# Optimization experiments

Hardware: AMD Instinct MI355X
Metric: run time of the kernel (lower is better)

The kernel has to match this reference:

```python
import jax, jax.numpy as jnp
import numpy as np

HIDDEN = 1024
NUM_QUBITS = 16
QUBIT_DIM = 64  # HIDDEN == NUM_QUBITS * QUBIT_DIM
LN_EPS = 1e-6   # flax nn.LayerNorm default


def setup_inputs() -> dict:
    key = jax.random.key(0)
    k_x, k_w = jax.random.split(key)
    B, S = 4, 4096
    x = jax.random.normal(k_x, (B, S, HIDDEN), dtype=jnp.float32)
    # Learned params (flax defaults: LN scale=ones, bias=zeros; Dense lecun_normal kernel, zero bias)
    ln_scale = jnp.ones((HIDDEN,), dtype=jnp.float32)
    ln_bias = jnp.zeros((HIDDEN,), dtype=jnp.float32)
    dense_w = jax.random.normal(k_w, (HIDDEN, HIDDEN), dtype=jnp.float32) * (1.0 / np.sqrt(HIDDEN))
    dense_b = jnp.zeros((HIDDEN,), dtype=jnp.float32)
    return {"x": x, "ln_scale": ln_scale, "ln_bias": ln_bias,
            "dense_w": dense_w, "dense_b": dense_b}


def reference(x, ln_scale, ln_bias, dense_w, dense_b):
    B, S, H = x.shape
    # input_preparation: LayerNorm over last axis, then reshape (B,S,Q,D)
    mean = jnp.mean(x, axis=-1, keepdims=True)
    var = jnp.mean(jnp.square(x - mean), axis=-1, keepdims=True)
    h = (x - mean) * jax.lax.rsqrt(var + LN_EPS) * ln_scale + ln_bias
    h = h.reshape(B, S, NUM_QUBITS, QUBIT_DIM)
    # quantum_forward (default jax backend): sin*cos, FFT along qubit axis, real part
    h = jnp.sin(h) * jnp.cos(h)
    h = jnp.real(jnp.fft.fft(h.astype(jnp.complex64), axis=-2))
    # post_process: restore (B,S,H) then Dense(hidden_size)
    h = h.reshape(B, S, H)
    return jnp.einsum('bsh,hk->bsk', h, dense_w) + dense_b
```

## Files before the change

### kernel.cpp

```cpp
#include <hip/hip_runtime.h>
#include <hip/hip_bf16.h>

#define HID 1024
#define NQ 16
#define QD 64
#define MROWS 16384

typedef __bf16 bf16;
typedef __bf16 bf16x8 __attribute__((ext_vector_type(8)));
typedef __bf16 bf16x4 __attribute__((ext_vector_type(4)));
typedef float f32x4 __attribute__((ext_vector_type(4)));

__global__ __launch_bounds__(256) void wt_k(const float* __restrict__ W,
                                            bf16* __restrict__ Wt) {
    int idx = blockIdx.x * 256 + threadIdx.x;
    int n = idx >> 6;
    int d = idx & 63;

    float w[16];
#pragma unroll
    for (int qp = 0; qp < 16; ++qp)
        w[qp] = W[(size_t)(qp * QD + d) * HID + n];

    const float ct[16] = {
        1.0f,  0.92387953f,  0.70710678f,  0.38268343f,
        0.0f, -0.38268343f, -0.70710678f, -0.92387953f,
       -1.0f, -0.92387953f, -0.70710678f, -0.38268343f,
        0.0f,  0.38268343f,  0.70710678f,  0.92387953f};

#pragma unroll
    for (int q = 0; q < 16; ++q) {
        float acc = 0.0f;
#pragma unroll
        for (int qp = 0; qp < 16; ++qp)
            acc += w[qp] * ct[(q * qp) & 15];
        Wt[(size_t)n * HID + q * QD + d] = (bf16)acc;
    }
}

__global__ __launch_bounds__(256) void prep_k(const float* __restrict__ x,
                                              const float* __restrict__ gamma,
                                              const float* __restrict__ beta,
                                              bf16* __restrict__ A) {
    int row = blockIdx.x;
    int t = threadIdx.x;
    const float4* xr = (const float4*)(x + (size_t)row * HID);
    float4 v = xr[t];

    float s  = v.x + v.y + v.z + v.w;
    float ss = v.x * v.x + v.y * v.y + v.z * v.z + v.w * v.w;
#pragma unroll
    for (int off = 32; off; off >>= 1) {
        s  += __shfl_down(s, off);
        ss += __shfl_down(ss, off);
    }
    __shared__ float red[8];
    int wv = t >> 6, ln = t & 63;
    if (ln == 0) { red[wv] = s; red[4 + wv] = ss; }
    __syncthreads();
    float Sm = red[0] + red[1] + red[2] + red[3];
    float Ss = red[4] + red[5] + red[6] + red[7];
    float mean = Sm * (1.0f / HID);
    float var  = Ss * (1.0f / HID) - mean * mean;
    float rstd = rsqrtf(var + 1e-6f);

    float4 g = ((const float4*)gamma)[t];
    float4 b = ((const float4*)beta)[t];

    float h0 = (v.x - mean) * rstd * g.x + b.x;
    float h1 = (v.y - mean) * rstd * g.y + b.y;
    float h2 = (v.z - mean) * rstd * g.z + b.z;
    float h3 = (v.w - mean) * rstd * g.w + b.w;

    bf16x4 o;
    o[0] = (bf16)(0.5f * __sinf(2.0f * h0));
    o[1] = (bf16)(0.5f * __sinf(2.0f * h1));
    o[2] = (bf16)(0.5f * __sinf(2.0f * h2));
    o[3] = (bf16)(0.5f * __sinf(2.0f * h3));
    ((bf16x4*)(A + (size_t)row * HID))[t] = o;
}

#define BM 256
#define BN 256
#define BK 64
#define NT (HID / BK)

#define MFMA(va, vb, vc) __builtin_amdgcn_mfma_f32_16x16x32_bf16(va, vb, vc, 0, 0, 0)

__global__ __launch_bounds__(512, 2) void gemm_k(const bf16* __restrict__ A,
                                                 const bf16* __restrict__ Bt,
                                                 const float* __restrict__ bias,
                                                 float* __restrict__ C) {
    __shared__ __attribute__((aligned(16))) char lds[131072];

    const int tid = threadIdx.x;
    const int w = tid >> 6, ln = tid & 63;
    const int wm = w >> 2, wn = w & 3;
    const int fr = ln & 15, fq = ln >> 4;

    int orig = blockIdx.x;
    int wg = (orig & 7) * 32 + (orig >> 3);
    int bm = wg >> 2, bn = wg & 3;

    const bf16* Ab = A + (size_t)bm * BM * HID;
    const bf16* Bb = Bt + (size_t)bn * BN * HID;

    auto stage = [&](int buf, int mat, int R0, int kt) {
        const char* gsrc = (const char*)(mat ? Bb : Ab);
        char* base = lds + (((buf << 1) | mat) << 15) + (R0 << 7);
        const int kb = kt << 7;
#pragma unroll
        for (int l = 0; l < 2; ++l) {
            int c = (l << 9) + tid;
            int lr = c >> 3;
            int colB = ((c & 7) ^ (lr & 7)) << 4;
            const char* g = gsrc + (size_t)(R0 + lr) * (HID * 2) + kb + colB;
            __builtin_amdgcn_global_load_lds(
                (const __attribute__((address_space(1))) void*)g,
                (__attribute__((address_space(3))) void*)(base + (((l << 9) + (w << 6)) << 4)),
                16, 0, 0);
        }
    };

    auto readA = [&](int buf, int i, int ks) -> bf16x8 {
        int r = ((i * 2 + wm) << 4) + fr;
        int off = (r << 7) + (ks << 6) + (fq << 4);
        off ^= (fr & 7) << 4;
        return *(const bf16x8*)(lds + ((buf << 1) << 15) + off);
    };
    auto readB = [&](int buf, int j, int ks) -> bf16x8 {
        int r = ((j * 4 + wn) << 4) + fr;
        int off = (r << 7) + (ks << 6) + (fq << 4);
        off ^= (fr & 7) << 4;
        return *(const bf16x8*)(lds + (((buf << 1) | 1) << 15) + off);
    };

    f32x4 acc[8][4];
#pragma unroll
    for (int i = 0; i < 8; ++i)
#pragma unroll
        for (int j = 0; j < 4; ++j) acc[i][j] = (f32x4){0.f, 0.f, 0.f, 0.f};

    stage(0, 1, 0, 0);
    stage(0, 0, 128, 0);
    stage(0, 0, 0, 0);
    stage(0, 1, 128, 0);
    stage(1, 1, 0, 1);
    stage(1, 0, 128, 1);
    asm volatile("s_waitcnt vmcnt(4)" ::: "memory");
    __builtin_amdgcn_s_barrier();

    bf16x8 a[8][2], b[4][2];

#pragma unroll 1
    for (int t = 0; t < NT; ++t) {
        const int cur = t & 1, nxt = cur ^ 1;

#pragma unroll
        for (int i = 0; i < 4; ++i) { a[i][0] = readA(cur, i, 0); a[i][1] = readA(cur, i, 1); }
#pragma unroll
        for (int j = 0; j < 2; ++j) { b[j][0] = readB(cur, j, 0); b[j][1] = readB(cur, j, 1); }
        if (t + 1 < NT) stage(nxt, 0, 0, t + 1);
        __builtin_amdgcn_s_barrier();
        asm volatile("s_waitcnt lgkmcnt(0)" ::: "memory");
        __builtin_amdgcn_sched_barrier(0);
        __builtin_amdgcn_s_setprio(1);
#pragma unroll
        for (int i = 0; i < 4; ++i)
#pragma unroll
            for (int j = 0; j < 2; ++j) {
                acc[i][j] = MFMA(a[i][0], b[j][0], acc[i][j]);
                acc[i][j] = MFMA(a[i][1], b[j][1], acc[i][j]);
            }
        __builtin_amdgcn_s_setprio(0);
        __builtin_amdgcn_s_barrier();

#pragma unroll
        for (int i = 4; i < 8; ++i) { a[i][0] = readA(cur, i, 0); a[i][1] = readA(cur, i, 1); }
        if (t + 1 < NT) stage(nxt, 1, 128, t + 1);
        __builtin_amdgcn_s_barrier();
        asm volatile("s_waitcnt lgkmcnt(0)" ::: "memory");
        __builtin_amdgcn_sched_barrier(0);
        __builtin_amdgcn_s_setprio(1);
#pragma unroll
        for (int i = 4; i < 8; ++i)
#pragma unroll
            for (int j = 0; j < 2; ++j) {
                acc[i][j] = MFMA(a[i][0], b[j][0], acc[i][j]);
                acc[i][j] = MFMA(a[i][1], b[j][1], acc[i][j]);
            }
        __builtin_amdgcn_s_setprio(0);
        __builtin_amdgcn_s_barrier();

#pragma unroll
        for (int j = 2; j < 4; ++j) { b[j][0] = readB(cur, j, 0); b[j][1] = readB(cur, j, 1); }
        if (t + 2 < NT) stage(cur, 1, 0, t + 2);
        __builtin_amdgcn_s_barrier();
        asm volatile("s_waitcnt lgkmcnt(0)" ::: "memory");
        __builtin_amdgcn_sched_barrier(0);
        __builtin_amdgcn_s_setprio(1);
#pragma unroll
        for (int i = 4; i < 8; ++i)
#pragma unroll
            for (int j = 2; j < 4; ++j) {
                acc[i][j] = MFMA(a[i][0], b[j][0], acc[i][j]);
                acc[i][j] = MFMA(a[i][1], b[j][1], acc[i][j]);
            }
        __builtin_amdgcn_s_setprio(0);
        __builtin_amdgcn_s_barrier();

        if (t + 2 < NT) stage(cur, 0, 128, t + 2);
        __builtin_amdgcn_s_barrier();
        __builtin_amdgcn_s_setprio(1);
#pragma unroll
        for (int i = 0; i < 4; ++i)
#pragma unroll
            for (int j = 2; j < 4; ++j) {
                acc[i][j] = MFMA(a[i][0], b[j][0], acc[i][j]);
                acc[i][j] = MFMA(a[i][1], b[j][1], acc[i][j]);
            }
        __builtin_amdgcn_s_setprio(0);
        if (t + 2 < NT) {
            asm volatile("s_waitcnt vmcnt(4)" ::: "memory");
        } else if (t + 1 < NT) {
            asm volatile("s_waitcnt vmcnt(0)" ::: "memory");
        }
        __builtin_amdgcn_sched_barrier(0);
        __builtin_amdgcn_s_barrier();
    }

#pragma unroll
    for (int j = 0; j < 4; ++j) {
        int col = bn * BN + ((j * 4 + wn) << 4) + fr;
        float bv = bias[col];
#pragma unroll
        for (int i = 0; i < 8; ++i) {
            int row0 = bm * BM + ((i * 2 + wm) << 4) + (fq << 2);
#pragma unroll
            for (int jj = 0; jj < 4; ++jj)
                C[(size_t)(row0 + jj) * HID + col] = acc[i][j][jj] + bv;
        }
    }
}

extern "C" void kernel_launch(void* const* d_in, const int* in_sizes, int n_in,
                              void* d_out, int out_size, void* d_ws, size_t ws_size,
                              hipStream_t stream) {
    const float* x   = (const float*)d_in[0];
    const float* lng = (const float*)d_in[1];
    const float* lnb = (const float*)d_in[2];
    const float* W   = (const float*)d_in[3];
    const float* db  = (const float*)d_in[4];
    float* out = (float*)d_out;

    bf16* A  = (bf16*)d_ws;
    bf16* Wt = (bf16*)((char*)d_ws + (size_t)MROWS * HID * 2);

    wt_k<<<(HID * QD) / 256, 256, 0, stream>>>(W, Wt);
    prep_k<<<MROWS, 256, 0, stream>>>(x, lng, lnb, A);
    gemm_k<<<(MROWS / BM) * (HID / BN), 512, 0, stream>>>(A, Wt, db, out);
}
```

Baseline: 71.70 us.

## Load B operand directly from global into registers, stage only A in LDS

The GEMM now stages only the A tile in LDS, with BK raised to 128 and double buffering. Each wave loads its B fragments straight from global memory into registers with a two-deep register prefetch, which removes most barriers and the B LDS traffic. The weight transform kernel is also restructured to read W with coalesced float4 loads into a padded shared tile, replacing strided column reads. The risk is that B global loads now sit on the MFMA critical path, and 256KB of LDS with launch_bounds(512,2) may limit occupancy.

```diff
diff --git a/kernel.cpp b/kernel.cpp
--- a/kernel.cpp
+++ b/kernel.cpp
@@ -2,8 +2,6 @@
 #include <hip/hip_bf16.h>
 
 #define HID 1024
-#define NQ 16
-#define QD 64
 #define MROWS 16384
 
 typedef __bf16 bf16;
@@ -11,16 +9,25 @@
 typedef __bf16 bf16x4 __attribute__((ext_vector_type(4)));
 typedef float f32x4 __attribute__((ext_vector_type(4)));
 
+#define MFMA(va, vb, vc) __builtin_amdgcn_mfma_f32_16x16x32_bf16(va, vb, vc, 0, 0, 0)
+
 __global__ __launch_bounds__(256) void wt_k(const float* __restrict__ W,
                                             bf16* __restrict__ Wt) {
-    int idx = blockIdx.x * 256 + threadIdx.x;
-    int n = idx >> 6;
-    int d = idx & 63;
-
-    float w[16];
-#pragma unroll
-    for (int qp = 0; qp < 16; ++qp)
-        w[qp] = W[(size_t)(qp * QD + d) * HID + n];
+    __shared__ float Wl[1024][17];
+    const int tid = threadIdx.x;
+    const int n0 = blockIdx.x * 16;
+
+    {
+        int r = tid >> 2, nq = tid & 3;
+#pragma unroll
+        for (int p = 0; p < 16; ++p) {
+            int k = p * 64 + r;
+            float4 v = *(const float4*)&W[(size_t)k * HID + n0 + nq * 4];
+            Wl[k][nq * 4 + 0] = v.x; Wl[k][nq * 4 + 1] = v.y;
+            Wl[k][nq * 4 + 2] = v.z; Wl[k][nq * 4 + 3] = v.w;
+        }
+    }
+    __syncthreads();
 
     const float ct[16] = {
         1.0f,  0.92387953f,  0.70710678f,  0.38268343f,
@@ -28,13 +35,20 @@
        -1.0f, -0.92387953f, -0.70710678f, -0.38268343f,
         0.0f,  0.38268343f,  0.70710678f,  0.92387953f};
 
-#pragma unroll
-    for (int q = 0; q < 16; ++q) {
-        float acc = 0.0f;
-#pragma unroll
-        for (int qp = 0; qp < 16; ++qp)
-            acc += w[qp] * ct[(q * qp) & 15];
-        Wt[(size_t)n * HID + q * QD + d] = (bf16)acc;
+    const int d = tid & 63, ng = tid >> 6;
+#pragma unroll
+    for (int nn = 0; nn < 4; ++nn) {
+        int n = ng * 4 + nn;
+        float wv[16];
+#pragma unroll
+        for (int qp = 0; qp < 16; ++qp) wv[qp] = Wl[qp * 64 + d][n];
+#pragma unroll
+        for (int q = 0; q < 16; ++q) {
+            float acc = 0.0f;
+#pragma unroll
+            for (int qp = 0; qp < 16; ++qp) acc += wv[qp] * ct[(q * qp) & 15];
+            Wt[(size_t)(n0 + n) * HID + q * 64 + d] = (bf16)acc;
+        }
     }
 }
 
@@ -82,16 +96,14 @@
 
 #define BM 256
 #define BN 256
-#define BK 64
+#define BK 128
 #define NT (HID / BK)
-
-#define MFMA(va, vb, vc) __builtin_amdgcn_mfma_f32_16x16x32_bf16(va, vb, vc, 0, 0, 0)
 
 __global__ __launch_bounds__(512, 2) void gemm_k(const bf16* __restrict__ A,
                                                  const bf16* __restrict__ Bt,
                                                  const float* __restrict__ bias,
                                                  float* __restrict__ C) {
-    __shared__ __attribute__((aligned(16))) char lds[131072];
+    __shared__ __attribute__((aligned(16))) char sA[2][65536];
 
     const int tid = threadIdx.x;
     const int w = tid >> 6, ln = tid & 63;
@@ -100,39 +112,30 @@
 
     int orig = blockIdx.x;
     int wg = (orig & 7) * 32 + (orig >> 3);
-    int bm = wg >> 2, bn = wg & 3;
-
-    const bf16* Ab = A + (size_t)bm * BM * HID;
-    const bf16* Bb = Bt + (size_t)bn * BN * HID;
-
-    auto stage = [&](int buf, int mat, int R0, int kt) {
-        const char* gsrc = (const char*)(mat ? Bb : Ab);
-        char* base = lds + (((buf << 1) | mat) << 15) + (R0 << 7);
-        const int kb = kt << 7;
-#pragma unroll
-        for (int l = 0; l < 2; ++l) {
-            int c = (l << 9) + tid;
-            int lr = c >> 3;
-            int colB = ((c & 7) ^ (lr & 7)) << 4;
-            const char* g = gsrc + (size_t)(R0 + lr) * (HID * 2) + kb + colB;
-            __builtin_amdgcn_global_load_lds(
-                (const __attribute__((address_space(1))) void*)g,
-                (__attribute__((address_space(3))) void*)(base + (((l << 9) + (w << 6)) << 4)),
-                16, 0, 0);
-        }
+    const int bm = wg >> 2, bn = wg & 3;
+    const int m0 = bm * BM;
+    const int n0 = bn * BN + wn * 64;
+
+    auto stage = [&](int buf, int kt, int c) {
+        int lr = (c << 5) + (tid >> 4);
+        int sp = (tid & 15) ^ (lr & 7);
+        const char* g = (const char*)A + (size_t)(m0 + lr) * (HID * 2) +
+                        kt * (BK * 2) + (sp << 4);
+        char* d = sA[buf] + (c << 13) + (w << 10);
+        __builtin_amdgcn_global_load_lds(
+            (const __attribute__((address_space(1))) void*)g,
+            (__attribute__((address_space(3))) void*)d, 16, 0, 0);
     };
 
     auto readA = [&](int buf, int i, int ks) -> bf16x8 {
-        int r = ((i * 2 + wm) << 4) + fr;
-        int off = (r << 7) + (ks << 6) + (fq << 4);
-        off ^= (fr & 7) << 4;
-        return *(const bf16x8*)(lds + ((buf << 1) << 15) + off);
+        int row = wm * 128 + i * 16 + fr;
+        int off = (row << 8) + ((((ks << 2) | fq) ^ (fr & 7)) << 4);
+        return *(const bf16x8*)(sA[buf] + off);
     };
-    auto readB = [&](int buf, int j, int ks) -> bf16x8 {
-        int r = ((j * 4 + wn) << 4) + fr;
-        int off = (r << 7) + (ks << 6) + (fq << 4);
-        off ^= (fr & 7) << 4;
-        return *(const bf16x8*)(lds + (((buf << 1) | 1) << 15) + off);
+
+    auto loadB = [&](int kt, int ks, int j) -> bf16x8 {
+        return *(const bf16x8*)&Bt[(size_t)(n0 + (j << 4) + fr) * HID +
+                                   kt * BK + ks * 32 + (fq << 3)];
     };
 
     f32x4 acc[8][4];
@@ -141,104 +144,58 @@
 #pragma unroll
         for (int j = 0; j < 4; ++j) acc[i][j] = (f32x4){0.f, 0.f, 0.f, 0.f};
 
-    stage(0, 1, 0, 0);
-    stage(0, 0, 128, 0);
-    stage(0, 0, 0, 0);
-    stage(0, 1, 128, 0);
-    stage(1, 1, 0, 1);
-    stage(1, 0, 128, 1);
-    asm volatile("s_waitcnt vmcnt(4)" ::: "memory");
+#pragma unroll
+    for (int c = 0; c < 8; ++c) stage(0, 0, c);
+    bf16x8 b[2][4];
+#pragma unroll
+    for (int j = 0; j < 4; ++j) b[0][j] = loadB(0, 0, j);
+    asm volatile("s_waitcnt vmcnt(0)" ::: "memory");
     __builtin_amdgcn_s_barrier();
-
-    bf16x8 a[8][2], b[4][2];
 
 #pragma unroll 1
     for (int t = 0; t < NT; ++t) {
         const int cur = t & 1, nxt = cur ^ 1;
-
-#pragma unroll
-        for (int i = 0; i < 4; ++i) { a[i][0] = readA(cur, i, 0); a[i][1] = readA(cur, i, 1); }
-#pragma unroll
-        for (int j = 0; j < 2; ++j) { b[j][0] = readB(cur, j, 0); b[j][1] = readB(cur, j, 1); }
-        if (t + 1 < NT) stage(nxt, 0, 0, t + 1);
-        __builtin_amdgcn_s_barrier();
-        asm volatile("s_waitcnt lgkmcnt(0)" ::: "memory");
-        __builtin_amdgcn_sched_barrier(0);
-        __builtin_amdgcn_s_setprio(1);
-#pragma unroll
-        for (int i = 0; i < 4; ++i)
-#pragma unroll
-            for (int j = 0; j < 2; ++j) {
-                acc[i][j] = MFMA(a[i][0], b[j][0], acc[i][j]);
-                acc[i][j] = MFMA(a[i][1], b[j][1], acc[i][j]);
+#pragma unroll
+        for (int ks = 0; ks < 4; ++ks) {
+            if (t + 1 < NT) {
+                stage(nxt, t + 1, ks * 2);
+                stage(nxt, t + 1, ks * 2 + 1);
             }
-        __builtin_amdgcn_s_setprio(0);
-        __builtin_amdgcn_s_barrier();
-
-#pragma unroll
-        for (int i = 4; i < 8; ++i) { a[i][0] = readA(cur, i, 0); a[i][1] = readA(cur, i, 1); }
-        if (t + 1 < NT) stage(nxt, 1, 128, t + 1);
-        __builtin_amdgcn_s_barrier();
-        asm volatile("s_waitcnt lgkmcnt(0)" ::: "memory");
-        __builtin_amdgcn_sched_barrier(0);
-        __builtin_amdgcn_s_setprio(1);
-#pragma unroll
-        for (int i = 4; i < 8; ++i)
-#pragma unroll
-            for (int j = 0; j < 2; ++j) {
-                acc[i][j] = MFMA(a[i][0], b[j][0], acc[i][j]);
-                acc[i][j] = MFMA(a[i][1], b[j][1], acc[i][j]);
+            const int pb = ks & 1, pn = pb ^ 1;
+            if (!(t == NT - 1 && ks == 3)) {
+                const int tn = (ks == 3) ? t + 1 : t;
+                const int ksn = (ks + 1) & 3;
+#pragma unroll
+                for (int j = 0; j < 4; ++j) b[pn][j] = loadB(tn, ksn, j);
             }
-        __builtin_amdgcn_s_setprio(0);
-        __builtin_amdgcn_s_barrier();
-
-#pragma unroll
-        for (int j = 2; j < 4; ++j) { b[j][0] = readB(cur, j, 0); b[j][1] = readB(cur, j, 1); }
-        if (t + 2 < NT) stage(cur, 1, 0, t + 2);
-        __builtin_amdgcn_s_barrier();
-        asm volatile("s_waitcnt lgkmcnt(0)" ::: "memory");
-        __builtin_amdgcn_sched_barrier(0);
-        __builtin_amdgcn_s_setprio(1);
-#pragma unroll
-        for (int i = 4; i < 8; ++i)
-#pragma unroll
-            for (int j = 2; j < 4; ++j) {
-                acc[i][j] = MFMA(a[i][0], b[j][0], acc[i][j]);
-                acc[i][j] = MFMA(a[i][1], b[j][1], acc[i][j]);
-            }
-        __builtin_amdgcn_s_setprio(0);
-        __builtin_amdgcn_s_barrier();
-
-        if (t + 2 < NT) stage(cur, 0, 128, t + 2);
-        __builtin_amdgcn_s_barrier();
-        __builtin_amdgcn_s_setprio(1);
-#pragma unroll
-        for (int i = 0; i < 4; ++i)
-#pragma unroll
-            for (int j = 2; j < 4; ++j) {
-                acc[i][j] = MFMA(a[i][0], b[j][0], acc[i][j]);
-                acc[i][j] = MFMA(a[i][1], b[j][1], acc[i][j]);
-            }
-        __builtin_amdgcn_s_setprio(0);
-        if (t + 2 < NT) {
-            asm volatile("s_waitcnt vmcnt(4)" ::: "memory");
-        } else if (t + 1 < NT) {
+            bf16x8 a[8];
+#pragma unroll
+            for (int i = 0; i < 8; ++i) a[i] = readA(cur, i, ks);
+
+            __builtin_amdgcn_s_setprio(1);
+#pragma unroll
+            for (int i = 0; i < 8; ++i)
+#pragma unroll
+                for (int j = 0; j < 4; ++j)
+                    acc[i][j] = MFMA(a[i], b[pb][j], acc[i][j]);
+            __builtin_amdgcn_s_setprio(0);
+        }
+        if (t + 1 < NT) {
             asm volatile("s_waitcnt vmcnt(0)" ::: "memory");
-        }
-        __builtin_amdgcn_sched_barrier(0);
-        __builtin_amdgcn_s_barrier();
+            __builtin_amdgcn_s_barrier();
+        }
     }
 
 #pragma unroll
     for (int j = 0; j < 4; ++j) {
-        int col = bn * BN + ((j * 4 + wn) << 4) + fr;
+        int col = n0 + (j << 4) + fr;
         float bv = bias[col];
 #pragma unroll
         for (int i = 0; i < 8; ++i) {
-            int row0 = bm * BM + ((i * 2 + wm) << 4) + (fq << 2);
+            int r0 = m0 + wm * 128 + (i << 4) + (fq << 2);
 #pragma unroll
             for (int jj = 0; jj < 4; ++jj)
-                C[(size_t)(row0 + jj) * HID + col] = acc[i][j][jj] + bv;
+                C[(size_t)(r0 + jj) * HID + col] = acc[i][j][jj] + bv;
         }
     }
 }
@@ -256,7 +213,7 @@
     bf16* A  = (bf16*)d_ws;
     bf16* Wt = (bf16*)((char*)d_ws + (size_t)MROWS * HID * 2);
 
-    wt_k<<<(HID * QD) / 256, 256, 0, stream>>>(W, Wt);
+    wt_k<<<HID / 16, 256, 0, stream>>>(W, Wt);
     prep_k<<<MROWS, 256, 0, stream>>>(x, lng, lnb, A);
     gemm_k<<<(MROWS / BM) * (HID / BN), 512, 0, stream>>>(A, Wt, db, out);
 }
```

Measured after the change: 89.24 us. 1.24x slower.
